# Optimization experiments

Hardware: AMD Instinct MI355X
Metric: run time of the kernel (lower is better)

The kernel has to match this reference:

```python
import jax, jax.numpy as jnp
import numpy as np

B, S, C, D = 128, 128, 128, 64
NQ, NT = 5000, 1441

def setup_inputs() -> dict:
    key = jax.random.key(0)
    ks = jax.random.split(key, 20)
    def xav(k, shape):
        fan_in, fan_out = shape[0], shape[1]
        lim = float(np.sqrt(6.0 / (fan_in + fan_out)))
        return jax.random.uniform(k, shape, jnp.float32, -lim, lim)
    return {
        'question_seq': jax.random.randint(ks[0], (B, S), 0, NQ),
        'correctness_seq': jax.random.randint(ks[1], (B, S), 0, 2),
        'interval_time_seq': jax.random.randint(ks[2], (B, S), 0, NT),
        'use_time_seq': jax.random.randint(ks[3], (B, S), 0, NT),
        'E_q': jax.random.normal(ks[4], (NQ, D), jnp.float32) * 0.05,
        'E_c': jax.random.normal(ks[5], (2, D), jnp.float32) * 0.05,
        'E_it': jax.random.normal(ks[6], (NT, D), jnp.float32) * 0.05,
        'E_at': jax.random.normal(ks[7], (NT, D), jnp.float32) * 0.05,
        'q_matrix': (jax.random.uniform(ks[8], (NQ, C)) < 0.1).astype(jnp.float32),
        'h0': xav(ks[9], (C, D)),
        'W1': xav(ks[10], (3 * D, D)), 'b1': jnp.zeros((D,), jnp.float32),
        'W2': xav(ks[11], (4 * D, D)), 'b2': jnp.zeros((D,), jnp.float32),
        'W3': xav(ks[12], (4 * D, D)), 'b3': jnp.zeros((D,), jnp.float32),
        'W4': xav(ks[13], (3 * D, D)), 'b4': jnp.zeros((D,), jnp.float32),
        'W5': xav(ks[14], (2 * D, D)), 'b5': jnp.zeros((D,), jnp.float32),
    }

def _lpkt_forward(question_seq, correctness_seq, interval_time_seq, use_time_seq,
                  E_q, E_c, E_it, E_at, q_matrix, h0,
                  W1, b1, W2, b2, W3, b3, W4, b4, W5, b5):
    dim_k = W1.shape[1]
    b, s = question_seq.shape
    e_emb = E_q[question_seq]            # [B,S,D]
    c_emb = E_c[correctness_seq]         # [B,S,D]
    it_emb = E_it[interval_time_seq]     # [B,S,D]
    at_emb = E_at[use_time_seq]          # [B,S,D]
    # all learning vectors (linear_1 over full sequence, as in original)
    all_learning = jnp.concatenate([e_emb, at_emb, c_emb], -1) @ W1 + b1  # [B,S,D]
    q_e_seq = q_matrix[question_seq]     # [B,S,C]

    h_pre0 = jnp.broadcast_to(h0, (b,) + h0.shape)                 # [B,C,D]
    h_tilde0 = q_e_seq[:, 0] @ h0                                  # [B,D] (h_pre is batch-replicated)
    learning0 = jnp.zeros((b, dim_k), all_learning.dtype)

    # time-major xs for t = 0 .. s-2
    xs = (jnp.swapaxes(q_e_seq[:, :-1], 0, 1),      # q_e at t
          jnp.swapaxes(q_e_seq[:, 1:], 0, 1),       # q_e at t+1
          jnp.swapaxes(it_emb[:, :-1], 0, 1),       # it at t
          jnp.swapaxes(all_learning[:, :-1], 0, 1), # learning at t
          jnp.swapaxes(e_emb[:, 1:], 0, 1))         # e embed at t+1

    def step(carry, x):
        h_pre, h_tilde_pre, learning_pre = carry
        q_e, q_e_next, it, learning, e_next = x
        x4 = jnp.concatenate([learning_pre, it, learning, h_tilde_pre], -1)   # [B,4D]
        learning_gain = jnp.tanh(x4 @ W2 + b2)
        gamma_l = jax.nn.sigmoid(x4 @ W3 + b3)
        LG = gamma_l * (learning_gain + 1.0) * 0.5                            # [B,D]
        LG_tilde = q_e[:, :, None] * LG[:, None, :]                           # [B,C,D] scatter to concepts
        c = q_e.shape[1]
        x3 = jnp.concatenate([h_pre,
                              jnp.broadcast_to(LG[:, None, :], (LG.shape[0], c, dim_k)),
                              jnp.broadcast_to(it[:, None, :], (it.shape[0], c, dim_k))], -1)
        gamma_f = jax.nn.sigmoid(x3 @ W4 + b4)                                # [B,C,D]
        h = LG_tilde + gamma_f * h_pre                                        # [B,C,D]
        h_tilde = jnp.einsum('bc,bcd->bd', q_e_next, h)                       # gather for next question
        y = jax.nn.sigmoid(jnp.concatenate([e_next, h_tilde], -1) @ W5 + b5).mean(-1)
        return (h, h_tilde, learning), y

    _, ys = jax.lax.scan(step, (h_pre0, h_tilde0, learning0), xs)  # ys: [S-1, B]
    pred = jnp.zeros((b, s), ys.dtype).at[:, 1:].set(jnp.swapaxes(ys, 0, 1))
    return pred

def reference(question_seq, correctness_seq, interval_time_seq, use_time_seq,
              E_q, E_c, E_it, E_at, q_matrix, h0,
              W1, b1, W2, b2, W3, b3, W4, b4, W5, b5):
    return _lpkt_forward(question_seq, correctness_seq, interval_time_seq, use_time_seq,
                         E_q, E_c, E_it, E_at, q_matrix, h0,
                         W1, b1, W2, b2, W3, b3, W4, b4, W5, b5)
```

## Files before the change

### kernel.cpp

```cpp
#include <hip/hip_runtime.h>
#include <hip/hip_bf16.h>


#define NB 128
#define NS 128
#define NC 128
#define ND 64
#define POS (NB*NS)

typedef __attribute__((ext_vector_type(8))) short short8;
typedef __attribute__((ext_vector_type(4))) float f32x4;

__device__ __forceinline__ float rl(float v,int j){
  return __int_as_float(__builtin_amdgcn_readlane(__float_as_int(v), j));
}
#define HBF(c, d) ((((c)<<6) + (d)) ^ (((c)&7)<<3))
#define DPP_ADD(v, CTRL) ((v) + __int_as_float(__builtin_amdgcn_update_dpp(0, __float_as_int(v), CTRL, 0xF, 0xF, true)))
#define DPP_ROWSUM(v) do { v = DPP_ADD(v,0x111); v = DPP_ADD(v,0x112); v = DPP_ADD(v,0x114); v = DPP_ADD(v,0x118); } while(0)

#define SC1 (-1.4426950408889634f)

__device__ __forceinline__ float gsig(float zp){
  return __builtin_amdgcn_rcpf(1.f + __builtin_amdgcn_exp2f(zp));
}

__global__ __launch_bounds__(64) void lpkt_pre1(
    const int* __restrict__ qseq, const int* __restrict__ cseq,
    const int* __restrict__ itseq, const int* __restrict__ atseq,
    const float* __restrict__ E_q, const float* __restrict__ E_c,
    const float* __restrict__ E_it, const float* __restrict__ E_at,
    const float* __restrict__ W1, const float* __restrict__ b1,
    const float* __restrict__ W4, const float* __restrict__ b4,
    const float* __restrict__ W5, const float* __restrict__ b5,
    float* __restrict__ AL, float* __restrict__ pre4, float* __restrict__ pre5)
{
  __shared__ float sx[4][192];
  __shared__ float sit[4][64];
  const int d = threadIdx.x;
  #pragma unroll
  for (int i = 0; i < 4; ++i) {
    int p = blockIdx.x + i*4096;
    sx[i][d]      = E_q[qseq[p]*ND + d];
    sx[i][64+d]   = E_at[atseq[p]*ND + d];
    sx[i][128+d]  = E_c[cseq[p]*ND + d];
    sit[i][d]     = E_it[itseq[p]*ND + d];
  }
  __syncthreads();
  float al[4], p4[4], p5[4];
  const float b1d = b1[d], b4d = b4[d], b5d = b5[d];
  #pragma unroll
  for (int i = 0; i < 4; ++i) { al[i] = b1d; p4[i] = b4d; p5[i] = b5d; }
  for (int k = 0; k < 192; ++k) {
    float wv = W1[k*ND + d];
    #pragma unroll
    for (int i = 0; i < 4; ++i) al[i] = fmaf(sx[i][k], wv, al[i]);
  }
  for (int k = 0; k < 64; ++k) {
    float wv4 = W4[(128+k)*ND + d];
    float wv5 = W5[k*ND + d];
    #pragma unroll
    for (int i = 0; i < 4; ++i) {
      p4[i] = fmaf(sit[i][k], wv4, p4[i]);
      p5[i] = fmaf(sx[i][k],  wv5, p5[i]);
    }
  }
  #pragma unroll
  for (int i = 0; i < 4; ++i) {
    int p = blockIdx.x + i*4096;
    AL[p*ND + d]   = al[i];
    pre4[p*ND + d] = p4[i]*SC1;
    pre5[p*ND + d] = p5[i]*SC1;
  }
}

__global__ __launch_bounds__(64) void lpkt_pre2(
    const int* __restrict__ itseq, const float* __restrict__ E_it,
    const float* __restrict__ AL,
    const float* __restrict__ W2, const float* __restrict__ b2,
    const float* __restrict__ W3, const float* __restrict__ b3,
    float* __restrict__ pre2, float* __restrict__ pre3)
{
  __shared__ float sx[4][192];
  const int d = threadIdx.x;
  int bs4[4];
  #pragma unroll
  for (int i = 0; i < 4; ++i) {
    int p = blockIdx.x + i*4064;
    int b = p / 127;
    int t = p - b*127;
    int bs = b*NS + t;
    bs4[i] = bs;
    sx[i][d]     = (t > 0) ? AL[(bs-1)*ND + d] : 0.f;
    sx[i][64+d]  = E_it[itseq[bs]*ND + d];
    sx[i][128+d] = AL[bs*ND + d];
  }
  __syncthreads();
  float a2[4], a3[4];
  const float b2d = b2[d], b3d = b3[d];
  #pragma unroll
  for (int i = 0; i < 4; ++i) { a2[i] = b2d; a3[i] = b3d; }
  for (int k = 0; k < 192; ++k) {
    float w2v = W2[k*ND + d];
    float w3v = W3[k*ND + d];
    #pragma unroll
    for (int i = 0; i < 4; ++i) {
      a2[i] = fmaf(sx[i][k], w2v, a2[i]);
      a3[i] = fmaf(sx[i][k], w3v, a3[i]);
    }
  }
  #pragma unroll
  for (int i = 0; i < 4; ++i) {
    pre2[bs4[i]*ND + d] = a2[i]*(2.f*SC1);
    pre3[bs4[i]*ND + d] = a3[i]*SC1;
  }
}

__global__ __attribute__((amdgpu_flat_work_group_size(512,512), amdgpu_waves_per_eu(2,2)))
void lpkt_seq(
    const int* __restrict__ qseq, const float* __restrict__ qmat,
    const float* __restrict__ h0,
    const float* __restrict__ W2, const float* __restrict__ W3,
    const float* __restrict__ W4, const float* __restrict__ W5,
    const float* __restrict__ pre2, const float* __restrict__ pre3,
    const float* __restrict__ pre4, const float* __restrict__ pre5,
    float* __restrict__ out)
{
  __shared__ __align__(16) unsigned short sh_hbf[NC*ND];
  __shared__ float sh_pre[32][4][64];
  __shared__ float sh_qf[32][NC];
  __shared__ float sh_htp[4][64];
  __shared__ float sh_LG[64];
  __shared__ float sh_lgp[2][64];
  __shared__ float sh_out[NS];

  const int tid = threadIdx.x;
  const int w = tid>>6, l = tid&63;
  const int g = l>>4, li = l&15;
  const int b = blockIdx.x;
  const int Wq = w & 3, mm = (w>>2)*2;

  if (w==4 || w==5) __builtin_amdgcn_s_setprio(1);

  short8 aW[2][2];
  #pragma unroll
  for (int mloc=0;mloc<2;++mloc)
    #pragma unroll
    for (int k0=0;k0<2;++k0){
      short8 v;
      #pragma unroll
      for (int j=0;j<8;++j){
        __hip_bfloat16 hb = __float2bfloat16(W4[(32*k0+8*g+j)*ND + 16*(mm+mloc)+li] * SC1);
        v[j] = *(short*)&hb;
      }
      aW[mloc][k0] = v;
    }

  float ws2[64], ws3[64], wsB[32];
  if (w==4 || w==5){
    #pragma unroll
    for (int j=0;j<64;++j) ws2[j] = W2[(192+j)*ND + l] * (2.f*SC1);
    #pragma unroll
    for (int j=0;j<64;++j) ws3[j] = W3[(192+j)*ND + l] * SC1;
    const float* pb = W4 + ((w==4)?64:96)*ND;
    #pragma unroll
    for (int j=0;j<32;++j) wsB[j] = pb[j*ND + l] * SC1;
  } else if (w==6){
    #pragma unroll
    for (int j=0;j<64;++j) ws2[j] = W5[(64+j)*ND + l] * SC1;
  }

  float hreg[2][2][4];
  int wofs[2][2], bfofs[2][2];
  #pragma unroll
  for (int mloc=0;mloc<2;++mloc)
    #pragma unroll
    for (int t2=0;t2<2;++t2){
      int c  = 32*Wq + 16*t2 + li;
      int d0 = 16*(mm+mloc) + 4*g;
      wofs[t2][mloc] = HBF(c, d0);
      float4 v = *(const float4*)&h0[c*ND + d0];
      hreg[mloc][t2][0]=v.x; hreg[mloc][t2][1]=v.y;
      hreg[mloc][t2][2]=v.z; hreg[mloc][t2][3]=v.w;
      __hip_bfloat162 c01 = __float22bfloat162_rn(make_float2(v.x,v.y));
      __hip_bfloat162 c23 = __float22bfloat162_rn(make_float2(v.z,v.w));
      uint2 pk; pk.x = *(unsigned*)&c01; pk.y = *(unsigned*)&c23;
      *(uint2*)&sh_hbf[wofs[t2][mloc]] = pk;
    }
  #pragma unroll
  for (int t2=0;t2<2;++t2)
    #pragma unroll
    for (int k0=0;k0<2;++k0)
      bfofs[t2][k0] = HBF(32*Wq+16*t2+li, 32*k0+8*g);

  #pragma unroll
  for (int k2=0;k2<2;++k2){
    int f4id = tid + k2*512;
    if (f4id < 17*32){
      int r = f4id >> 5, c4 = (f4id & 31)*4;
      int qrow = qseq[b*NS + r];
      float4 v = *(const float4*)&qmat[qrow*NC + c4];
      *(float4*)&sh_qf[r][c4] = v;
    }
  }
  #pragma unroll
  for (int k2=0;k2<2;++k2){
    int f4id = tid + k2*512;
    int u = f4id >> 6;
    int inner = f4id & 63;
    int s = inner >> 4, c4 = (inner & 15)*4;
    const float* ps = (s==0)?pre2:(s==1)?pre3:(s==2)?pre4:pre5;
    float4 v = *(const float4*)&ps[(size_t)(b*NS+u)*ND + c4];
    *(float4*)(&sh_pre[u][0][0] + inner*4) = v;
  }
  if (tid==0) sh_out[0] = 0.f;
  __syncthreads();

  {
    float part[2][4] = {{0.f,0.f,0.f,0.f},{0.f,0.f,0.f,0.f}};
    #pragma unroll
    for (int t2=0;t2<2;++t2){
      float qv = sh_qf[0][32*Wq+16*t2+li];
      #pragma unroll
      for (int mloc=0;mloc<2;++mloc)
        #pragma unroll
        for (int r2=0;r2<4;++r2)
          part[mloc][r2] = fmaf(qv, hreg[mloc][t2][r2], part[mloc][r2]);
    }
    #pragma unroll
    for (int mloc=0;mloc<2;++mloc)
      #pragma unroll
      for (int r2=0;r2<4;++r2){ float v=part[mloc][r2]; DPP_ROWSUM(v); part[mloc][r2]=v; }
    if (li==15){
      #pragma unroll
      for (int mloc=0;mloc<2;++mloc){
        float4 pv; pv.x=part[mloc][0]; pv.y=part[mloc][1]; pv.z=part[mloc][2]; pv.w=part[mloc][3];
        *(float4*)&sh_htp[Wq][16*(mm+mloc)+4*g] = pv;
      }
    }
  }
  __syncthreads();

  float qc0 = sh_qf[0][32*Wq+li];
  float qc1 = sh_qf[0][32*Wq+16+li];

  const float* prebase;
  { int s = l>>4;
    const float* ps = (s==0)?pre2:(s==1)?pre3:(s==2)?pre4:pre5;
    prebase = ps + (size_t)(b*NS)*ND + (l&15)*4; }

  for (int t=0; t<127; ++t){
    const int slot = t & 31, sn = (t+1) & 31;

    f32x4 acc[2][2];
    #pragma unroll
    for (int mloc=0;mloc<2;++mloc)
      #pragma unroll
      for (int t2=0;t2<2;++t2)
        acc[mloc][t2] = (f32x4){0.f,0.f,0.f,0.f};
    #pragma unroll
    for (int t2=0;t2<2;++t2){
      #pragma unroll
      for (int k0=0;k0<2;++k0){
        short8 bf = *(const short8*)&sh_hbf[bfofs[t2][k0]];
        acc[0][t2] = __builtin_amdgcn_mfma_f32_16x16x32_bf16(aW[0][k0], bf, acc[0][t2], 0,0,0);
        acc[1][t2] = __builtin_amdgcn_mfma_f32_16x16x32_bf16(aW[1][k0], bf, acc[1][t2], 0,0,0);
      }
    }
    float qn0 = sh_qf[sn][32*Wq+li];
    float qn1 = sh_qf[sn][32*Wq+16+li];

    if (w==4 || w==5){
      float htv = (sh_htp[0][l]+sh_htp[1][l])+(sh_htp[2][l]+sh_htp[3][l]);
      float pv2 = sh_pre[slot][0][l], pv3 = sh_pre[slot][1][l];
      float a0=pv2,a1=0.f,a2_=0.f,a3_=0.f;
      float c0=pv3,c1=0.f,c2_=0.f,c3_=0.f;
      #pragma unroll
      for (int j=0;j<64;j+=4){
        float h0_=rl(htv,j), h1_=rl(htv,j+1), h2_=rl(htv,j+2), h3_=rl(htv,j+3);
        a0 =fmaf(h0_,ws2[j  ],a0 ); c0 =fmaf(h0_,ws3[j  ],c0 );
        a1 =fmaf(h1_,ws2[j+1],a1 ); c1 =fmaf(h1_,ws3[j+1],c1 );
        a2_=fmaf(h2_,ws2[j+2],a2_); c2_=fmaf(h2_,ws3[j+2],c2_);
        a3_=fmaf(h3_,ws2[j+3],a3_); c3_=fmaf(h3_,ws3[j+3],c3_);
      }
      float a2p=(a0+a1)+(a2_+a3_), a3p=(c0+c1)+(c2_+c3_);
      float LGl = gsig(a3p) * gsig(a2p);
      if (w==4){
        sh_LG[l] = LGl;
        float e0=sh_pre[slot][2][l],e1=0.f,e2=0.f,e3=0.f;
        #pragma unroll
        for (int j=0;j<32;j+=4){
          e0=fmaf(rl(LGl,j  ),wsB[j  ],e0); e1=fmaf(rl(LGl,j+1),wsB[j+1],e1);
          e2=fmaf(rl(LGl,j+2),wsB[j+2],e2); e3=fmaf(rl(LGl,j+3),wsB[j+3],e3);
        }
        sh_lgp[0][l] = (e0+e1)+(e2+e3);
      } else {
        float e0=0.f,e1=0.f,e2=0.f,e3=0.f;
        #pragma unroll
        for (int j=0;j<32;j+=4){
          e0=fmaf(rl(LGl,32+j  ),wsB[j  ],e0); e1=fmaf(rl(LGl,32+j+1),wsB[j+1],e1);
          e2=fmaf(rl(LGl,32+j+2),wsB[j+2],e2); e3=fmaf(rl(LGl,32+j+3),wsB[j+3],e3);
        }
        sh_lgp[1][l] = (e0+e1)+(e2+e3);
      }
    } else if (w==6){
      if (t > 0){
        float htv = (sh_htp[0][l]+sh_htp[1][l])+(sh_htp[2][l]+sh_htp[3][l]);
        float z0=sh_pre[slot][3][l],z1=0.f,z2=0.f,z3=0.f;
        #pragma unroll
        for (int j=0;j<64;j+=4){
          z0=fmaf(rl(htv,j  ),ws2[j  ],z0); z1=fmaf(rl(htv,j+1),ws2[j+1],z1);
          z2=fmaf(rl(htv,j+2),ws2[j+2],z2); z3=fmaf(rl(htv,j+3),ws2[j+3],z3);
        }
        float yv = gsig((z0+z1)+(z2+z3));
        DPP_ROWSUM(yv);
        float s = (rl(yv,15)+rl(yv,31))+(rl(yv,47)+rl(yv,63));
        if (l==0) sh_out[t] = s*(1.f/64.f);
      }
    } else if (w==3){
      if ((t&15)==0){
        int t0r = t+17;
        #pragma unroll
        for (int rep=0; rep<8; ++rep){
          int f4id = rep*64 + l;
          int r = t0r + (f4id>>5);
          int c4 = (f4id & 31)*4;
          if (r < NS){
            int qrow = qseq[b*NS + r];
            float4 v = *(const float4*)&qmat[qrow*NC + c4];
            *(float4*)&sh_qf[r&31][c4] = v;
          }
        }
      }
    } else if (w==7){
      if ((t&15)==0){
        #pragma unroll
        for (int rep=0; rep<16; ++rep){
          int u = t+16+rep;
          if (u < NS){
            float4 v = *(const float4*)&prebase[(size_t)u*ND];
            *(float4*)(&sh_pre[u&31][0][0] + l*4) = v;
          }
        }
      }
    }
    __syncthreads();

    {
      float4 LG4[2]; float gi[2][4];
      #pragma unroll
      for (int mloc=0;mloc<2;++mloc){
        int d0 = 16*(mm+mloc)+4*g;
        LG4[mloc] = *(const float4*)&sh_LG[d0];
        float4 g0v = *(const float4*)&sh_lgp[0][d0];
        float4 g1v = *(const float4*)&sh_lgp[1][d0];
        gi[mloc][0]=g0v.x+g1v.x; gi[mloc][1]=g0v.y+g1v.y;
        gi[mloc][2]=g0v.z+g1v.z; gi[mloc][3]=g0v.w+g1v.w;
      }
      float part[2][4] = {{0.f,0.f,0.f,0.f},{0.f,0.f,0.f,0.f}};
      #pragma unroll
      for (int t2=0;t2<2;++t2){
        float qcv = t2 ? qc1 : qc0;
        float qnv = t2 ? qn1 : qn0;
        #pragma unroll
        for (int mloc=0;mloc<2;++mloc){
          float lg4a[4] = {LG4[mloc].x, LG4[mloc].y, LG4[mloc].z, LG4[mloc].w};
          float hn[4];
          #pragma unroll
          for (int r2=0;r2<4;++r2){
            float gam = gsig(acc[mloc][t2][r2] + gi[mloc][r2]);
            hn[r2] = fmaf(qcv, lg4a[r2], gam*hreg[mloc][t2][r2]);
            hreg[mloc][t2][r2] = hn[r2];
            part[mloc][r2] = fmaf(qnv, hn[r2], part[mloc][r2]);
          }
          __hip_bfloat162 c01 = __float22bfloat162_rn(make_float2(hn[0],hn[1]));
          __hip_bfloat162 c23 = __float22bfloat162_rn(make_float2(hn[2],hn[3]));
          uint2 pk; pk.x=*(unsigned*)&c01; pk.y=*(unsigned*)&c23;
          *(uint2*)&sh_hbf[wofs[t2][mloc]] = pk;
        }
      }
      #pragma unroll
      for (int mloc=0;mloc<2;++mloc)
        #pragma unroll
        for (int r2=0;r2<4;++r2){ float v=part[mloc][r2]; DPP_ROWSUM(v); part[mloc][r2]=v; }
      if (li==15){
        #pragma unroll
        for (int mloc=0;mloc<2;++mloc){
          float4 pv; pv.x=part[mloc][0]; pv.y=part[mloc][1]; pv.z=part[mloc][2]; pv.w=part[mloc][3];
          *(float4*)&sh_htp[Wq][16*(mm+mloc)+4*g] = pv;
        }
      }
      qc0 = qn0; qc1 = qn1;
    }
    __syncthreads();
  }

  if (w==6){
    float htv = (sh_htp[0][l]+sh_htp[1][l])+(sh_htp[2][l]+sh_htp[3][l]);
    float z0=sh_pre[31][3][l],z1=0.f,z2=0.f,z3=0.f;
    #pragma unroll
    for (int j=0;j<64;j+=4){
      z0=fmaf(rl(htv,j  ),ws2[j  ],z0); z1=fmaf(rl(htv,j+1),ws2[j+1],z1);
      z2=fmaf(rl(htv,j+2),ws2[j+2],z2); z3=fmaf(rl(htv,j+3),ws2[j+3],z3);
    }
    float yv = gsig((z0+z1)+(z2+z3));
    DPP_ROWSUM(yv);
    float s = (rl(yv,15)+rl(yv,31))+(rl(yv,47)+rl(yv,63));
    if (l==0) sh_out[127] = s*(1.f/64.f);
  }
  __syncthreads();
  if (tid < NS) out[b*NS + tid] = sh_out[tid];
}

extern "C" void kernel_launch(void* const* d_in, const int* in_sizes, int n_in,
                              void* d_out, int out_size, void* d_ws, size_t ws_size,
                              hipStream_t stream)
{
  const int*   qseq  = (const int*)d_in[0];
  const int*   cseq  = (const int*)d_in[1];
  const int*   itseq = (const int*)d_in[2];
  const int*   atseq = (const int*)d_in[3];
  const float* E_q   = (const float*)d_in[4];
  const float* E_c   = (const float*)d_in[5];
  const float* E_it  = (const float*)d_in[6];
  const float* E_at  = (const float*)d_in[7];
  const float* qmat  = (const float*)d_in[8];
  const float* h0    = (const float*)d_in[9];
  const float* W1    = (const float*)d_in[10];
  const float* b1    = (const float*)d_in[11];
  const float* W2    = (const float*)d_in[12];
  const float* b2    = (const float*)d_in[13];
  const float* W3    = (const float*)d_in[14];
  const float* b3    = (const float*)d_in[15];
  const float* W4    = (const float*)d_in[16];
  const float* b4    = (const float*)d_in[17];
  const float* W5    = (const float*)d_in[18];
  const float* b5    = (const float*)d_in[19];
  float* out = (float*)d_out;

  float* wsf  = (float*)d_ws;
  float* AL   = wsf;
  float* pre2 = wsf + 1*POS*ND;
  float* pre3 = wsf + 2*POS*ND;
  float* pre4 = wsf + 3*POS*ND;
  float* pre5 = wsf + 4*POS*ND;

  lpkt_pre1<<<4096, 64, 0, stream>>>(qseq, cseq, itseq, atseq,
                                     E_q, E_c, E_it, E_at,
                                     W1, b1, W4, b4, W5, b5,
                                     AL, pre4, pre5);
  lpkt_pre2<<<4064, 64, 0, stream>>>(itseq, E_it, AL, W2, b2, W3, b3, pre2, pre3);
  lpkt_seq<<<128, 512, 0, stream>>>(qseq, qmat, h0, W2, W3, W4, W5,
                                    pre2, pre3, pre4, pre5, out);
}
```

Before: 289.8 us.

## Reassociate h_tilde projections as MFMA over the bf16 knowledge state

Instead of first reducing h_tilde = q·h and then running serial readlane/FMA dot products on two waves, every wave now multiplies its bf16 h tiles by the W2, W3 and W5 slices using MFMA, then applies q-weighted DPP reductions into shared partial sums. The LG contribution to the forget gate is also done by MFMA, with LG packed to bf16 in shared memory, rather than scalar wsB loops. This removes the long serial scalar chain on a few waves from the per-step critical path. In exchange it adds more MFMAs, another barrier per step, more register pressure from five weight fragment sets, and bf16 rounding on paths that were previously fp32.

Result: slower. 350.3 us (+20.9%).

```diff
diff --git a/kernel.cpp b/kernel.cpp
--- a/kernel.cpp
+++ b/kernel.cpp
@@ -115,7 +115,37 @@
   }
 }
 
-__global__ __attribute__((amdgpu_flat_work_group_size(512,512), amdgpu_waves_per_eu(2,2)))
+#define MM4(accM, aWM) do {                                                     \
+  _Pragma("unroll")                                                             \
+  for (int mloc_=0;mloc_<2;++mloc_)                                             \
+    _Pragma("unroll")                                                           \
+    for (int t2_=0;t2_<2;++t2_){                                                \
+      accM[mloc_][t2_] = __builtin_amdgcn_mfma_f32_16x16x32_bf16(aWM[mloc_][0], bfr[t2_][0], accM[mloc_][t2_],0,0,0); \
+      accM[mloc_][t2_] = __builtin_amdgcn_mfma_f32_16x16x32_bf16(aWM[mloc_][1], bfr[t2_][1], accM[mloc_][t2_],0,0,0); \
+    }                                                                           \
+} while(0)
+
+#define QREDUCE(accM, shP) do {                                                 \
+  float pv_[2][4];                                                              \
+  _Pragma("unroll")                                                             \
+  for (int mloc_=0;mloc_<2;++mloc_)                                             \
+    _Pragma("unroll")                                                           \
+    for (int r2_=0;r2_<4;++r2_){                                                \
+      float v_ = fmaf(qc1, accM[mloc_][1][r2_], qc0*accM[mloc_][0][r2_]);       \
+      DPP_ROWSUM(v_);                                                           \
+      pv_[mloc_][r2_] = v_;                                                     \
+    }                                                                           \
+  if (li==15){                                                                  \
+    _Pragma("unroll")                                                           \
+    for (int mloc_=0;mloc_<2;++mloc_){                                          \
+      float4 f_; f_.x=pv_[mloc_][0]; f_.y=pv_[mloc_][1];                        \
+      f_.z=pv_[mloc_][2]; f_.w=pv_[mloc_][3];                                   \
+      *(float4*)&shP[Wq][16*(mm+mloc_)+4*g] = f_;                               \
+    }                                                                           \
+  }                                                                             \
+} while(0)
+
+__global__ __launch_bounds__(512) __attribute__((amdgpu_waves_per_eu(2)))
 void lpkt_seq(
     const int* __restrict__ qseq, const float* __restrict__ qmat,
     const float* __restrict__ h0,
@@ -128,9 +158,11 @@
   __shared__ __align__(16) unsigned short sh_hbf[NC*ND];
   __shared__ float sh_pre[32][4][64];
   __shared__ float sh_qf[32][NC];
-  __shared__ float sh_htp[4][64];
+  __shared__ float sh_p2[4][64];
+  __shared__ float sh_p3[4][64];
+  __shared__ float sh_p5[4][64];
   __shared__ float sh_LG[64];
-  __shared__ float sh_lgp[2][64];
+  __shared__ __align__(16) unsigned sh_LGb[32];
   __shared__ float sh_out[NS];
 
   const int tid = threadIdx.x;
@@ -139,35 +171,29 @@
   const int b = blockIdx.x;
   const int Wq = w & 3, mm = (w>>2)*2;
 
-  if (w==4 || w==5) __builtin_amdgcn_s_setprio(1);
-
-  short8 aW[2][2];
+  if (w==4) __builtin_amdgcn_s_setprio(1);
+
+  short8 aW2[2][2], aW3[2][2], aW4[2][2], aW5[2][2], aW4b[2][2];
   #pragma unroll
   for (int mloc=0;mloc<2;++mloc)
     #pragma unroll
     for (int k0=0;k0<2;++k0){
-      short8 v;
+      short8 v2,v3,v4,v5,vb;
       #pragma unroll
       for (int j=0;j<8;++j){
-        __hip_bfloat16 hb = __float2bfloat16(W4[(32*k0+8*g+j)*ND + 16*(mm+mloc)+li] * SC1);
-        v[j] = *(short*)&hb;
-      }
-      aW[mloc][k0] = v;
-    }
-
-  float ws2[64], ws3[64], wsB[32];
-  if (w==4 || w==5){
-    #pragma unroll
-    for (int j=0;j<64;++j) ws2[j] = W2[(192+j)*ND + l] * (2.f*SC1);
-    #pragma unroll
-    for (int j=0;j<64;++j) ws3[j] = W3[(192+j)*ND + l] * SC1;
-    const float* pb = W4 + ((w==4)?64:96)*ND;
-    #pragma unroll
-    for (int j=0;j<32;++j) wsB[j] = pb[j*ND + l] * SC1;
-  } else if (w==6){
-    #pragma unroll
-    for (int j=0;j<64;++j) ws2[j] = W5[(64+j)*ND + l] * SC1;
-  }
+        int k = 32*k0 + 8*g + j;
+        int dc = 16*(mm+mloc) + li;
+        __hip_bfloat16 h2 = __float2bfloat16(W2[(192+k)*ND + dc] * (2.f*SC1));
+        __hip_bfloat16 h3 = __float2bfloat16(W3[(192+k)*ND + dc] * SC1);
+        __hip_bfloat16 h4 = __float2bfloat16(W4[k*ND        + dc] * SC1);
+        __hip_bfloat16 h5 = __float2bfloat16(W5[(64+k)*ND  + dc] * SC1);
+        __hip_bfloat16 hb = __float2bfloat16(W4[(64+k)*ND  + dc] * SC1);
+        v2[j]=*(short*)&h2; v3[j]=*(short*)&h3; v4[j]=*(short*)&h4;
+        v5[j]=*(short*)&h5; vb[j]=*(short*)&hb;
+      }
+      aW2[mloc][k0]=v2; aW3[mloc][k0]=v3; aW4[mloc][k0]=v4;
+      aW5[mloc][k0]=v5; aW4b[mloc][k0]=vb;
+    }
 
   float hreg[2][2][4];
   int wofs[2][2], bfofs[2][2];
@@ -215,31 +241,6 @@
   if (tid==0) sh_out[0] = 0.f;
   __syncthreads();
 
-  {
-    float part[2][4] = {{0.f,0.f,0.f,0.f},{0.f,0.f,0.f,0.f}};
-    #pragma unroll
-    for (int t2=0;t2<2;++t2){
-      float qv = sh_qf[0][32*Wq+16*t2+li];
-      #pragma unroll
-      for (int mloc=0;mloc<2;++mloc)
-        #pragma unroll
-        for (int r2=0;r2<4;++r2)
-          part[mloc][r2] = fmaf(qv, hreg[mloc][t2][r2], part[mloc][r2]);
-    }
-    #pragma unroll
-    for (int mloc=0;mloc<2;++mloc)
-      #pragma unroll
-      for (int r2=0;r2<4;++r2){ float v=part[mloc][r2]; DPP_ROWSUM(v); part[mloc][r2]=v; }
-    if (li==15){
-      #pragma unroll
-      for (int mloc=0;mloc<2;++mloc){
-        float4 pv; pv.x=part[mloc][0]; pv.y=part[mloc][1]; pv.z=part[mloc][2]; pv.w=part[mloc][3];
-        *(float4*)&sh_htp[Wq][16*(mm+mloc)+4*g] = pv;
-      }
-    }
-  }
-  __syncthreads();
-
   float qc0 = sh_qf[0][32*Wq+li];
   float qc1 = sh_qf[0][32*Wq+16+li];
 
@@ -251,67 +252,57 @@
   for (int t=0; t<127; ++t){
     const int slot = t & 31, sn = (t+1) & 31;
 
-    f32x4 acc[2][2];
-    #pragma unroll
-    for (int mloc=0;mloc<2;++mloc)
-      #pragma unroll
-      for (int t2=0;t2<2;++t2)
-        acc[mloc][t2] = (f32x4){0.f,0.f,0.f,0.f};
-    #pragma unroll
-    for (int t2=0;t2<2;++t2){
-      #pragma unroll
-      for (int k0=0;k0<2;++k0){
-        short8 bf = *(const short8*)&sh_hbf[bfofs[t2][k0]];
-        acc[0][t2] = __builtin_amdgcn_mfma_f32_16x16x32_bf16(aW[0][k0], bf, acc[0][t2], 0,0,0);
-        acc[1][t2] = __builtin_amdgcn_mfma_f32_16x16x32_bf16(aW[1][k0], bf, acc[1][t2], 0,0,0);
-      }
-    }
-    float qn0 = sh_qf[sn][32*Wq+li];
-    float qn1 = sh_qf[sn][32*Wq+16+li];
-
-    if (w==4 || w==5){
-      float htv = (sh_htp[0][l]+sh_htp[1][l])+(sh_htp[2][l]+sh_htp[3][l]);
-      float pv2 = sh_pre[slot][0][l], pv3 = sh_pre[slot][1][l];
-      float a0=pv2,a1=0.f,a2_=0.f,a3_=0.f;
-      float c0=pv3,c1=0.f,c2_=0.f,c3_=0.f;
-      #pragma unroll
-      for (int j=0;j<64;j+=4){
-        float h0_=rl(htv,j), h1_=rl(htv,j+1), h2_=rl(htv,j+2), h3_=rl(htv,j+3);
-        a0 =fmaf(h0_,ws2[j  ],a0 ); c0 =fmaf(h0_,ws3[j  ],c0 );
-        a1 =fmaf(h1_,ws2[j+1],a1 ); c1 =fmaf(h1_,ws3[j+1],c1 );
-        a2_=fmaf(h2_,ws2[j+2],a2_); c2_=fmaf(h2_,ws3[j+2],c2_);
-        a3_=fmaf(h3_,ws2[j+3],a3_); c3_=fmaf(h3_,ws3[j+3],c3_);
-      }
-      float a2p=(a0+a1)+(a2_+a3_), a3p=(c0+c1)+(c2_+c3_);
+    short8 bfr[2][2];
+    #pragma unroll
+    for (int t2=0;t2<2;++t2)
+      #pragma unroll
+      for (int k0=0;k0<2;++k0)
+        bfr[t2][k0] = *(const short8*)&sh_hbf[bfofs[t2][k0]];
+
+    f32x4 acc4[2][2];
+    {
+      f32x4 acc2[2][2], acc3[2][2];
+      #pragma unroll
+      for (int i=0;i<2;++i)
+        #pragma unroll
+        for (int j2=0;j2<2;++j2){
+          acc2[i][j2]=(f32x4){0.f,0.f,0.f,0.f};
+          acc3[i][j2]=(f32x4){0.f,0.f,0.f,0.f};
+        }
+      MM4(acc2, aW2);
+      MM4(acc3, aW3);
+      QREDUCE(acc2, sh_p2);
+      QREDUCE(acc3, sh_p3);
+    }
+    {
+      f32x4 acc5[2][2];
+      #pragma unroll
+      for (int i=0;i<2;++i)
+        #pragma unroll
+        for (int j2=0;j2<2;++j2){
+          acc5[i][j2]=(f32x4){0.f,0.f,0.f,0.f};
+          acc4[i][j2]=(f32x4){0.f,0.f,0.f,0.f};
+        }
+      MM4(acc5, aW5);
+      MM4(acc4, aW4);
+      QREDUCE(acc5, sh_p5);
+    }
+    __syncthreads();
+
+    if (w==4){
+      float a2p = ((sh_p2[0][l]+sh_p2[1][l])+(sh_p2[2][l]+sh_p2[3][l])) + sh_pre[slot][0][l];
+      float a3p = ((sh_p3[0][l]+sh_p3[1][l])+(sh_p3[2][l]+sh_p3[3][l])) + sh_pre[slot][1][l];
       float LGl = gsig(a3p) * gsig(a2p);
-      if (w==4){
-        sh_LG[l] = LGl;
-        float e0=sh_pre[slot][2][l],e1=0.f,e2=0.f,e3=0.f;
-        #pragma unroll
-        for (int j=0;j<32;j+=4){
-          e0=fmaf(rl(LGl,j  ),wsB[j  ],e0); e1=fmaf(rl(LGl,j+1),wsB[j+1],e1);
-          e2=fmaf(rl(LGl,j+2),wsB[j+2],e2); e3=fmaf(rl(LGl,j+3),wsB[j+3],e3);
-        }
-        sh_lgp[0][l] = (e0+e1)+(e2+e3);
-      } else {
-        float e0=0.f,e1=0.f,e2=0.f,e3=0.f;
-        #pragma unroll
-        for (int j=0;j<32;j+=4){
-          e0=fmaf(rl(LGl,32+j  ),wsB[j  ],e0); e1=fmaf(rl(LGl,32+j+1),wsB[j+1],e1);
-          e2=fmaf(rl(LGl,32+j+2),wsB[j+2],e2); e3=fmaf(rl(LGl,32+j+3),wsB[j+3],e3);
-        }
-        sh_lgp[1][l] = (e0+e1)+(e2+e3);
+      sh_LG[l] = LGl;
+      float nb = __int_as_float(__builtin_amdgcn_update_dpp(0, __float_as_int(LGl), 0xB1, 0xF, 0xF, true));
+      if (!(l&1)){
+        __hip_bfloat162 pk = __float22bfloat162_rn(make_float2(LGl, nb));
+        sh_LGb[l>>1] = *(unsigned*)&pk;
       }
     } else if (w==6){
       if (t > 0){
-        float htv = (sh_htp[0][l]+sh_htp[1][l])+(sh_htp[2][l]+sh_htp[3][l]);
-        float z0=sh_pre[slot][3][l],z1=0.f,z2=0.f,z3=0.f;
-        #pragma unroll
-        for (int j=0;j<64;j+=4){
-          z0=fmaf(rl(htv,j  ),ws2[j  ],z0); z1=fmaf(rl(htv,j+1),ws2[j+1],z1);
-          z2=fmaf(rl(htv,j+2),ws2[j+2],z2); z3=fmaf(rl(htv,j+3),ws2[j+3],z3);
-        }
-        float yv = gsig((z0+z1)+(z2+z3));
+        float z = ((sh_p5[0][l]+sh_p5[1][l])+(sh_p5[2][l]+sh_p5[3][l])) + sh_pre[slot][3][l];
+        float yv = gsig(z);
         DPP_ROWSUM(yv);
         float s = (rl(yv,15)+rl(yv,31))+(rl(yv,47)+rl(yv,63));
         if (l==0) sh_out[t] = s*(1.f/64.f);
@@ -346,31 +337,41 @@
     __syncthreads();
 
     {
-      float4 LG4[2]; float gi[2][4];
+      short8 lgb[2];
+      #pragma unroll
+      for (int k0=0;k0<2;++k0)
+        lgb[k0] = *(const short8*)((const char*)sh_LGb + 64*k0 + 16*g);
+      #pragma unroll
+      for (int mloc=0;mloc<2;++mloc)
+        #pragma unroll
+        for (int t2=0;t2<2;++t2){
+          acc4[mloc][t2] = __builtin_amdgcn_mfma_f32_16x16x32_bf16(aW4b[mloc][0], lgb[0], acc4[mloc][t2],0,0,0);
+          acc4[mloc][t2] = __builtin_amdgcn_mfma_f32_16x16x32_bf16(aW4b[mloc][1], lgb[1], acc4[mloc][t2],0,0,0);
+        }
+
+      float lg4a[2][4], p44[2][4];
       #pragma unroll
       for (int mloc=0;mloc<2;++mloc){
         int d0 = 16*(mm+mloc)+4*g;
-        LG4[mloc] = *(const float4*)&sh_LG[d0];
-        float4 g0v = *(const float4*)&sh_lgp[0][d0];
-        float4 g1v = *(const float4*)&sh_lgp[1][d0];
-        gi[mloc][0]=g0v.x+g1v.x; gi[mloc][1]=g0v.y+g1v.y;
-        gi[mloc][2]=g0v.z+g1v.z; gi[mloc][3]=g0v.w+g1v.w;
-      }
-      float part[2][4] = {{0.f,0.f,0.f,0.f},{0.f,0.f,0.f,0.f}};
+        float4 lg = *(const float4*)&sh_LG[d0];
+        float4 p4 = *(const float4*)&sh_pre[slot][2][d0];
+        lg4a[mloc][0]=lg.x; lg4a[mloc][1]=lg.y; lg4a[mloc][2]=lg.z; lg4a[mloc][3]=lg.w;
+        p44[mloc][0]=p4.x; p44[mloc][1]=p4.y; p44[mloc][2]=p4.z; p44[mloc][3]=p4.w;
+      }
+      float qn0 = sh_qf[sn][32*Wq+li];
+      float qn1 = sh_qf[sn][32*Wq+16+li];
+
       #pragma unroll
       for (int t2=0;t2<2;++t2){
         float qcv = t2 ? qc1 : qc0;
-        float qnv = t2 ? qn1 : qn0;
         #pragma unroll
         for (int mloc=0;mloc<2;++mloc){
-          float lg4a[4] = {LG4[mloc].x, LG4[mloc].y, LG4[mloc].z, LG4[mloc].w};
           float hn[4];
           #pragma unroll
           for (int r2=0;r2<4;++r2){
-            float gam = gsig(acc[mloc][t2][r2] + gi[mloc][r2]);
-            hn[r2] = fmaf(qcv, lg4a[r2], gam*hreg[mloc][t2][r2]);
+            float gam = gsig(acc4[mloc][t2][r2] + p44[mloc][r2]);
+            hn[r2] = fmaf(qcv, lg4a[mloc][r2], gam*hreg[mloc][t2][r2]);
             hreg[mloc][t2][r2] = hn[r2];
-            part[mloc][r2] = fmaf(qnv, hn[r2], part[mloc][r2]);
           }
           __hip_bfloat162 c01 = __float22bfloat162_rn(make_float2(hn[0],hn[1]));
           __hip_bfloat162 c23 = __float22bfloat162_rn(make_float2(hn[2],hn[3]));
@@ -378,31 +379,31 @@
           *(uint2*)&sh_hbf[wofs[t2][mloc]] = pk;
         }
       }
-      #pragma unroll
-      for (int mloc=0;mloc<2;++mloc)
-        #pragma unroll
-        for (int r2=0;r2<4;++r2){ float v=part[mloc][r2]; DPP_ROWSUM(v); part[mloc][r2]=v; }
-      if (li==15){
-        #pragma unroll
-        for (int mloc=0;mloc<2;++mloc){
-          float4 pv; pv.x=part[mloc][0]; pv.y=part[mloc][1]; pv.z=part[mloc][2]; pv.w=part[mloc][3];
-          *(float4*)&sh_htp[Wq][16*(mm+mloc)+4*g] = pv;
-        }
-      }
       qc0 = qn0; qc1 = qn1;
     }
     __syncthreads();
   }
 
+  {
+    short8 bfr[2][2];
+    #pragma unroll
+    for (int t2=0;t2<2;++t2)
+      #pragma unroll
+      for (int k0=0;k0<2;++k0)
+        bfr[t2][k0] = *(const short8*)&sh_hbf[bfofs[t2][k0]];
+    f32x4 acc5[2][2];
+    #pragma unroll
+    for (int i=0;i<2;++i)
+      #pragma unroll
+      for (int j2=0;j2<2;++j2)
+        acc5[i][j2]=(f32x4){0.f,0.f,0.f,0.f};
+    MM4(acc5, aW5);
+    QREDUCE(acc5, sh_p5);
+  }
+  __syncthreads();
   if (w==6){
-    float htv = (sh_htp[0][l]+sh_htp[1][l])+(sh_htp[2][l]+sh_htp[3][l]);
-    float z0=sh_pre[31][3][l],z1=0.f,z2=0.f,z3=0.f;
-    #pragma unroll
-    for (int j=0;j<64;j+=4){
-      z0=fmaf(rl(htv,j  ),ws2[j  ],z0); z1=fmaf(rl(htv,j+1),ws2[j+1],z1);
-      z2=fmaf(rl(htv,j+2),ws2[j+2],z2); z3=fmaf(rl(htv,j+3),ws2[j+3],z3);
-    }
-    float yv = gsig((z0+z1)+(z2+z3));
+    float z = ((sh_p5[0][l]+sh_p5[1][l])+(sh_p5[2][l]+sh_p5[3][l])) + sh_pre[31][3][l];
+    float yv = gsig(z);
     DPP_ROWSUM(yv);
     float s = (rl(yv,15)+rl(yv,31))+(rl(yv,47)+rl(yv,63));
     if (l==0) sh_out[127] = s*(1.f/64.f);
```

## Use packed fp16 dot2 for recurrent matvecs and defer MFMA after serial work

Applied to the files above, without the earlier changes.

The per-step matvecs in the critical serial waves (gates from h_tilde, the forget-gate partial, and the output projection) now keep weights as packed fp16 pairs and use v_dot2 with half as many readlanes. A DPP swap builds adjacent-lane pairs. The MFMA for the gamma pre-activation is moved after each wave's role-specific work, so the serial chain starts sooner. The launch attribute changes from waves_per_eu to launch_bounds, and register use drops. The fp16 rounding of weights and activations may reduce accuracy.

Measured after the change: 278.1 us. -4.0%, faster.

```diff
diff --git a/kernel.cpp b/kernel.cpp
--- a/kernel.cpp
+++ b/kernel.cpp
@@ -10,10 +10,31 @@
 
 typedef __attribute__((ext_vector_type(8))) short short8;
 typedef __attribute__((ext_vector_type(4))) float f32x4;
+typedef __attribute__((ext_vector_type(2))) _Float16 half2_t;
 
 __device__ __forceinline__ float rl(float v,int j){
   return __int_as_float(__builtin_amdgcn_readlane(__float_as_int(v), j));
 }
+__device__ __forceinline__ half2_t rlh2(half2_t v,int j){
+  int x; __builtin_memcpy(&x,&v,4);
+  x = __builtin_amdgcn_readlane(x,j);
+  half2_t r; __builtin_memcpy(&r,&x,4); return r;
+}
+__device__ __forceinline__ half2_t pkrtz(float a, float b){
+  auto t = __builtin_amdgcn_cvt_pkrtz(a,b);
+  half2_t r; __builtin_memcpy(&r,&t,4); return r;
+}
+__device__ __forceinline__ float dppswap(float v){
+  return __int_as_float(__builtin_amdgcn_update_dpp(0,__float_as_int(v),0xB1,0xF,0xF,true));
+}
+__device__ __forceinline__ float dot2h(half2_t a, half2_t b, float c){
+#if __has_builtin(__builtin_amdgcn_fdot2)
+  return __builtin_amdgcn_fdot2(a,b,c,false);
+#else
+  return fmaf((float)a[0],(float)b[0], fmaf((float)a[1],(float)b[1], c));
+#endif
+}
+
 #define HBF(c, d) ((((c)<<6) + (d)) ^ (((c)&7)<<3))
 #define DPP_ADD(v, CTRL) ((v) + __int_as_float(__builtin_amdgcn_update_dpp(0, __float_as_int(v), CTRL, 0xF, 0xF, true)))
 #define DPP_ROWSUM(v) do { v = DPP_ADD(v,0x111); v = DPP_ADD(v,0x112); v = DPP_ADD(v,0x114); v = DPP_ADD(v,0x118); } while(0)
@@ -115,7 +136,26 @@
   }
 }
 
-__global__ __attribute__((amdgpu_flat_work_group_size(512,512), amdgpu_waves_per_eu(2,2)))
+#define LOADB() do {                                                         \
+  _Pragma("unroll")                                                          \
+  for (int t2_=0;t2_<2;++t2_)                                                \
+    _Pragma("unroll")                                                        \
+    for (int k0_=0;k0_<2;++k0_)                                              \
+      bfr[t2_][k0_] = *(const short8*)&sh_hbf[bfofs[t2_][k0_]];              \
+} while(0)
+
+#define MFMA8() do {                                                         \
+  _Pragma("unroll")                                                          \
+  for (int t2_=0;t2_<2;++t2_){                                               \
+    _Pragma("unroll")                                                        \
+    for (int k0_=0;k0_<2;++k0_){                                             \
+      acc[0][t2_] = __builtin_amdgcn_mfma_f32_16x16x32_bf16(aW[0][k0_], bfr[t2_][k0_], acc[0][t2_],0,0,0); \
+      acc[1][t2_] = __builtin_amdgcn_mfma_f32_16x16x32_bf16(aW[1][k0_], bfr[t2_][k0_], acc[1][t2_],0,0,0); \
+    }                                                                        \
+  }                                                                          \
+} while(0)
+
+__global__ __launch_bounds__(512)
 void lpkt_seq(
     const int* __restrict__ qseq, const float* __restrict__ qmat,
     const float* __restrict__ h0,
@@ -155,18 +195,21 @@
       aW[mloc][k0] = v;
     }
 
-  float ws2[64], ws3[64], wsB[32];
+  half2_t wA[32], wB[32], wC[16];
   if (w==4 || w==5){
     #pragma unroll
-    for (int j=0;j<64;++j) ws2[j] = W2[(192+j)*ND + l] * (2.f*SC1);
-    #pragma unroll
-    for (int j=0;j<64;++j) ws3[j] = W3[(192+j)*ND + l] * SC1;
+    for (int j=0;j<32;++j){
+      wA[j] = pkrtz(W2[(192+2*j)*ND + l]*(2.f*SC1), W2[(193+2*j)*ND + l]*(2.f*SC1));
+      wB[j] = pkrtz(W3[(192+2*j)*ND + l]*SC1,       W3[(193+2*j)*ND + l]*SC1);
+    }
     const float* pb = W4 + ((w==4)?64:96)*ND;
     #pragma unroll
-    for (int j=0;j<32;++j) wsB[j] = pb[j*ND + l] * SC1;
+    for (int j=0;j<16;++j)
+      wC[j] = pkrtz(pb[(2*j)*ND + l]*SC1, pb[(2*j+1)*ND + l]*SC1);
   } else if (w==6){
     #pragma unroll
-    for (int j=0;j<64;++j) ws2[j] = W5[(64+j)*ND + l] * SC1;
+    for (int j=0;j<32;++j)
+      wA[j] = pkrtz(W5[(64+2*j)*ND + l]*SC1, W5[(65+2*j)*ND + l]*SC1);
   }
 
   float hreg[2][2][4];
@@ -257,65 +300,57 @@
       #pragma unroll
       for (int t2=0;t2<2;++t2)
         acc[mloc][t2] = (f32x4){0.f,0.f,0.f,0.f};
-    #pragma unroll
-    for (int t2=0;t2<2;++t2){
-      #pragma unroll
-      for (int k0=0;k0<2;++k0){
-        short8 bf = *(const short8*)&sh_hbf[bfofs[t2][k0]];
-        acc[0][t2] = __builtin_amdgcn_mfma_f32_16x16x32_bf16(aW[0][k0], bf, acc[0][t2], 0,0,0);
-        acc[1][t2] = __builtin_amdgcn_mfma_f32_16x16x32_bf16(aW[1][k0], bf, acc[1][t2], 0,0,0);
-      }
-    }
-    float qn0 = sh_qf[sn][32*Wq+li];
-    float qn1 = sh_qf[sn][32*Wq+16+li];
+    short8 bfr[2][2];
 
     if (w==4 || w==5){
+      float pv2 = sh_pre[slot][0][l], pv3 = sh_pre[slot][1][l];
       float htv = (sh_htp[0][l]+sh_htp[1][l])+(sh_htp[2][l]+sh_htp[3][l]);
-      float pv2 = sh_pre[slot][0][l], pv3 = sh_pre[slot][1][l];
-      float a0=pv2,a1=0.f,a2_=0.f,a3_=0.f;
-      float c0=pv3,c1=0.f,c2_=0.f,c3_=0.f;
-      #pragma unroll
-      for (int j=0;j<64;j+=4){
-        float h0_=rl(htv,j), h1_=rl(htv,j+1), h2_=rl(htv,j+2), h3_=rl(htv,j+3);
-        a0 =fmaf(h0_,ws2[j  ],a0 ); c0 =fmaf(h0_,ws3[j  ],c0 );
-        a1 =fmaf(h1_,ws2[j+1],a1 ); c1 =fmaf(h1_,ws3[j+1],c1 );
-        a2_=fmaf(h2_,ws2[j+2],a2_); c2_=fmaf(h2_,ws3[j+2],c2_);
-        a3_=fmaf(h3_,ws2[j+3],a3_); c3_=fmaf(h3_,ws3[j+3],c3_);
-      }
-      float a2p=(a0+a1)+(a2_+a3_), a3p=(c0+c1)+(c2_+c3_);
-      float LGl = gsig(a3p) * gsig(a2p);
+      half2_t hpk = pkrtz(htv, dppswap(htv));
+      float a20=pv2, a21=0.f, a30=pv3, a31=0.f;
+      #pragma unroll
+      for (int j=0;j<32;j+=2){
+        half2_t ha = rlh2(hpk, 2*j), hb = rlh2(hpk, 2*j+2);
+        a20 = dot2h(ha, wA[j],   a20); a21 = dot2h(hb, wA[j+1], a21);
+        a30 = dot2h(ha, wB[j],   a30); a31 = dot2h(hb, wB[j+1], a31);
+      }
+      float LGl = gsig(a30+a31) * gsig(a20+a21);
+      half2_t LGpk = pkrtz(LGl, dppswap(LGl));
       if (w==4){
         sh_LG[l] = LGl;
-        float e0=sh_pre[slot][2][l],e1=0.f,e2=0.f,e3=0.f;
-        #pragma unroll
-        for (int j=0;j<32;j+=4){
-          e0=fmaf(rl(LGl,j  ),wsB[j  ],e0); e1=fmaf(rl(LGl,j+1),wsB[j+1],e1);
-          e2=fmaf(rl(LGl,j+2),wsB[j+2],e2); e3=fmaf(rl(LGl,j+3),wsB[j+3],e3);
-        }
-        sh_lgp[0][l] = (e0+e1)+(e2+e3);
+        float e0 = sh_pre[slot][2][l], e1 = 0.f;
+        #pragma unroll
+        for (int j=0;j<16;j+=2){
+          e0 = dot2h(rlh2(LGpk, 2*j),   wC[j],   e0);
+          e1 = dot2h(rlh2(LGpk, 2*j+2), wC[j+1], e1);
+        }
+        sh_lgp[0][l] = e0+e1;
       } else {
-        float e0=0.f,e1=0.f,e2=0.f,e3=0.f;
-        #pragma unroll
-        for (int j=0;j<32;j+=4){
-          e0=fmaf(rl(LGl,32+j  ),wsB[j  ],e0); e1=fmaf(rl(LGl,32+j+1),wsB[j+1],e1);
-          e2=fmaf(rl(LGl,32+j+2),wsB[j+2],e2); e3=fmaf(rl(LGl,32+j+3),wsB[j+3],e3);
-        }
-        sh_lgp[1][l] = (e0+e1)+(e2+e3);
-      }
+        float e0 = 0.f, e1 = 0.f;
+        #pragma unroll
+        for (int j=0;j<16;j+=2){
+          e0 = dot2h(rlh2(LGpk, 32+2*j),   wC[j],   e0);
+          e1 = dot2h(rlh2(LGpk, 32+2*j+2), wC[j+1], e1);
+        }
+        sh_lgp[1][l] = e0+e1;
+      }
+      LOADB(); MFMA8();
     } else if (w==6){
       if (t > 0){
+        float pv5 = sh_pre[slot][3][l];
         float htv = (sh_htp[0][l]+sh_htp[1][l])+(sh_htp[2][l]+sh_htp[3][l]);
-        float z0=sh_pre[slot][3][l],z1=0.f,z2=0.f,z3=0.f;
-        #pragma unroll
-        for (int j=0;j<64;j+=4){
-          z0=fmaf(rl(htv,j  ),ws2[j  ],z0); z1=fmaf(rl(htv,j+1),ws2[j+1],z1);
-          z2=fmaf(rl(htv,j+2),ws2[j+2],z2); z3=fmaf(rl(htv,j+3),ws2[j+3],z3);
-        }
-        float yv = gsig((z0+z1)+(z2+z3));
+        half2_t hpk = pkrtz(htv, dppswap(htv));
+        float z0 = pv5, z1 = 0.f;
+        #pragma unroll
+        for (int j=0;j<32;j+=2){
+          z0 = dot2h(rlh2(hpk, 2*j),   wA[j],   z0);
+          z1 = dot2h(rlh2(hpk, 2*j+2), wA[j+1], z1);
+        }
+        float yv = gsig(z0+z1);
         DPP_ROWSUM(yv);
         float s = (rl(yv,15)+rl(yv,31))+(rl(yv,47)+rl(yv,63));
         if (l==0) sh_out[t] = s*(1.f/64.f);
       }
+      LOADB(); MFMA8();
     } else if (w==3){
       if ((t&15)==0){
         int t0r = t+17;
@@ -331,6 +366,7 @@
           }
         }
       }
+      LOADB(); MFMA8();
     } else if (w==7){
       if ((t&15)==0){
         #pragma unroll
@@ -342,7 +378,12 @@
           }
         }
       }
-    }
+      LOADB(); MFMA8();
+    } else {
+      LOADB(); MFMA8();
+    }
+    float qn0 = sh_qf[sn][32*Wq+li];
+    float qn1 = sh_qf[sn][32*Wq+16+li];
     __syncthreads();
 
     {
@@ -396,13 +437,14 @@
 
   if (w==6){
     float htv = (sh_htp[0][l]+sh_htp[1][l])+(sh_htp[2][l]+sh_htp[3][l]);
-    float z0=sh_pre[31][3][l],z1=0.f,z2=0.f,z3=0.f;
-    #pragma unroll
-    for (int j=0;j<64;j+=4){
-      z0=fmaf(rl(htv,j  ),ws2[j  ],z0); z1=fmaf(rl(htv,j+1),ws2[j+1],z1);
-      z2=fmaf(rl(htv,j+2),ws2[j+2],z2); z3=fmaf(rl(htv,j+3),ws2[j+3],z3);
-    }
-    float yv = gsig((z0+z1)+(z2+z3));
+    half2_t hpk = pkrtz(htv, dppswap(htv));
+    float z0 = sh_pre[31][3][l], z1 = 0.f;
+    #pragma unroll
+    for (int j=0;j<32;j+=2){
+      z0 = dot2h(rlh2(hpk, 2*j),   wA[j],   z0);
+      z1 = dot2h(rlh2(hpk, 2*j+2), wA[j+1], z1);
+    }
+    float yv = gsig(z0+z1);
     DPP_ROWSUM(yv);
     float s = (rl(yv,15)+rl(yv,31))+(rl(yv,47)+rl(yv,63));
     if (l==0) sh_out[127] = s*(1.f/64.f);
```
